# Performance work log

Hardware: AMD Instinct MI355X
Metric: run time of the kernel (lower is better)

## Reference

```python
import jax, jax.numpy as jnp
import numpy as np

THRESHOLD = 0.5
NEG_POS_RATIO = 3
ALPHA = 1.0
B, P, C, O = 64, 8732, 81, 32


def setup_inputs() -> dict:
    key = jax.random.key(0)
    k1, k2, k3, k4, k5, k6 = jax.random.split(key, 6)
    pred_locs = jax.random.normal(k1, (B, P, 4), dtype=jnp.float32)
    pred_scores = jax.random.normal(k2, (B, P, C), dtype=jnp.float32)
    # valid ground-truth corner boxes: sample center/size, convert to xy, clip to [0,1]
    ctr = jax.random.uniform(k3, (B, O, 2), minval=0.1, maxval=0.9)
    wh = jax.random.uniform(k4, (B, O, 2), minval=0.05, maxval=0.4)
    boxes = jnp.clip(jnp.concatenate([ctr - wh / 2, ctr + wh / 2], axis=-1), 0.0, 1.0)
    labels = jax.random.randint(k5, (B, O), 1, C, dtype=jnp.int64)
    pc = jax.random.uniform(k6, (P, 2), minval=0.05, maxval=0.95)
    pwh = jax.random.uniform(jax.random.fold_in(k6, 1), (P, 2), minval=0.05, maxval=0.3)
    priors_cxcy = jnp.concatenate([pc, pwh], axis=-1)
    return {"pred_locs": pred_locs, "pred_scores": pred_scores,
            "boxes": boxes, "labels": labels, "priors_cxcy": priors_cxcy}


def _jaccard(b, priors_xy):
    # b: [O,4] xy, priors_xy: [P,4] xy -> [O,P]
    lo = jnp.maximum(b[:, None, :2], priors_xy[None, :, :2])
    hi = jnp.minimum(b[:, None, 2:], priors_xy[None, :, 2:])
    inter = jnp.prod(jnp.clip(hi - lo, 0.0), axis=-1)
    area_b = jnp.prod(b[:, 2:] - b[:, :2], axis=-1)
    area_p = jnp.prod(priors_xy[:, 2:] - priors_xy[:, :2], axis=-1)
    return inter / (area_b[:, None] + area_p[None, :] - inter)


def _forward(pred_locs, pred_scores, boxes, labels, priors_cxcy):
    priors_xy = jnp.concatenate([priors_cxcy[:, :2] - priors_cxcy[:, 2:] / 2,
                                 priors_cxcy[:, :2] + priors_cxcy[:, 2:] / 2], axis=1)
    n_obj = boxes.shape[1]

    def match(b, l):
        ov = _jaccard(b, priors_xy)                      # [O,P]
        ov_fp = jnp.max(ov, axis=0)                      # [P]
        obj_fp = jnp.argmax(ov, axis=0)                  # [P]
        prior_fo = jnp.argmax(ov, axis=1)                # [O]
        obj_fp = obj_fp.at[prior_fo].set(jnp.arange(n_obj))
        ov_fp = ov_fp.at[prior_fo].set(1.0)
        lab = jnp.where(ov_fp < THRESHOLD, 0, l[obj_fp]) # [P]
        pt = b[obj_fp]                                   # [P,4] xy
        c = jnp.concatenate([(pt[:, 2:] + pt[:, :2]) / 2, pt[:, 2:] - pt[:, :2]], axis=1)
        g = jnp.concatenate([(c[:, :2] - priors_cxcy[:, :2]) / (priors_cxcy[:, 2:] / 10),
                             jnp.log(c[:, 2:] / priors_cxcy[:, 2:]) * 5], axis=1)
        return g, lab

    true_locs, true_classes = jax.vmap(match)(boxes, labels)  # [B,P,4], [B,P]

    pos = true_classes != 0                                   # [B,P]
    n_pos = jnp.sum(pos, axis=1)                              # [B]
    n_pos_total = jnp.sum(n_pos).astype(pred_locs.dtype)

    # L1Loss (mean over positive elements, 4 coords each)
    loc_abs = jnp.abs(pred_locs - true_locs) * pos[..., None].astype(pred_locs.dtype)
    loc_loss = jnp.sum(loc_abs) / (n_pos_total * 4.0)

    # per-prior cross entropy
    logp = jax.nn.log_softmax(pred_scores, axis=-1)           # [B,P,C]
    ce = -jnp.take_along_axis(logp, true_classes[..., None], axis=-1)[..., 0]  # [B,P]

    posf = pos.astype(ce.dtype)
    conf_pos_sum = jnp.sum(ce * posf)
    conf_neg = jnp.where(pos, 0.0, ce)
    conf_neg_sorted = -jnp.sort(-conf_neg, axis=1)            # descending
    ranks = jnp.arange(ce.shape[1])[None, :]
    hard = ranks < (NEG_POS_RATIO * n_pos)[:, None]
    conf_hard_neg_sum = jnp.sum(conf_neg_sorted * hard.astype(ce.dtype))

    conf_loss = (conf_hard_neg_sum + conf_pos_sum) / n_pos_total
    return conf_loss + ALPHA * loc_loss


def reference(pred_locs, pred_scores, boxes, labels, priors_cxcy):
    return _forward(pred_locs, pred_scores, boxes, labels, priors_cxcy)
```

## Files before the change

kernel.cpp:

```cpp
#include <hip/hip_runtime.h>

#define BB 64
#define PP 8732
#define OO 32
#define CC 81
#define NEGPOS 3
#define NSL_A 18
#define NCH_B 32
#define CHB 273
#define NSL_C 8
#define SLC 1092
#define NCE 8732

#define WS_POVF   0
#define WS_POVO   (WS_POVF  + BB*PP*4)
#define WS_BESTP  (WS_POVO  + BB*PP)
#define WS_LAB    (WS_BESTP + BB*NCH_B*OO*8)
#define WS_CENEG  (WS_LAB   + BB*PP)
#define WS_CEPOS  (WS_CENEG + BB*PP*4)
#define WS_LSUMB  (WS_CEPOS + NCE*4)
#define WS_NPOSB  (WS_LSUMB + BB*NSL_C*4)
#define WS_HARDB  (WS_NPOSB + BB*NSL_C*4)
#define WS_DONE   (WS_HARDB + BB*4)

__global__ __launch_bounds__(512) void match_geom(
    const float* __restrict__ boxes, const float* __restrict__ priors,
    float* __restrict__ povf, unsigned char* __restrict__ povo,
    unsigned long long* __restrict__ bestp, int* __restrict__ done)
{
    const int b = blockIdx.y, gx = blockIdx.x, tid = threadIdx.x;
    __shared__ float sbx[OO * 4];
    __shared__ unsigned long long sred[8 * OO];
    if (tid < OO * 4) sbx[tid] = boxes[b * OO * 4 + tid];
    if (gx == 0 && b == 0 && tid == 0) *done = 0;
    __syncthreads();

    if (gx < NSL_A) {
        const int p = gx * 512 + tid;
        if (p >= PP) return;
        float4 pr = ((const float4*)priors)[p];
        float plx = pr.x - pr.z * 0.5f, ply = pr.y - pr.w * 0.5f;
        float phx = pr.x + pr.z * 0.5f, phy = pr.y + pr.w * 0.5f;
        float parea = pr.z * pr.w;
        float bestv = -1.0f; int besto = 0;
#pragma unroll
        for (int o = 0; o < OO; ++o) {
            float b0 = sbx[o*4+0], b1 = sbx[o*4+1], b2 = sbx[o*4+2], b3 = sbx[o*4+3];
            float lox = fmaxf(b0, plx), loy = fmaxf(b1, ply);
            float hix = fminf(b2, phx), hiy = fminf(b3, phy);
            float inter = fmaxf(hix - lox, 0.0f) * fmaxf(hiy - loy, 0.0f);
            float iou = inter / ((b2 - b0) * (b3 - b1) + parea - inter);
            if (iou > bestv) { bestv = iou; besto = o; }
        }
        povf[b * PP + p] = bestv;
        povo[b * PP + p] = (unsigned char)besto;
    } else {
        const int ch = gx - NSL_A;
        const int o = tid & 31, sub = tid >> 5;
        const float b0 = sbx[o*4+0], b1 = sbx[o*4+1], b2 = sbx[o*4+2], b3 = sbx[o*4+3];
        const float barea = (b2 - b0) * (b3 - b1);
        const int base = ch * CHB;
        unsigned long long best = 0ull;
        for (int i = sub; i < CHB; i += 16) {
            int p = base + i;
            if (p >= PP) break;
            float4 pr = ((const float4*)priors)[p];
            float plx = pr.x - pr.z * 0.5f, ply = pr.y - pr.w * 0.5f;
            float phx = pr.x + pr.z * 0.5f, phy = pr.y + pr.w * 0.5f;
            float parea = pr.z * pr.w;
            float lox = fmaxf(b0, plx), loy = fmaxf(b1, ply);
            float hix = fminf(b2, phx), hiy = fminf(b3, phy);
            float inter = fmaxf(hix - lox, 0.0f) * fmaxf(hiy - loy, 0.0f);
            float iou = inter / (barea + parea - inter);
            unsigned long long enc =
                ((unsigned long long)__float_as_uint(iou) << 32) | (unsigned)(~(unsigned)p);
            best = (enc > best) ? enc : best;
        }
        unsigned long long w = __shfl_down(best, 32, 64);
        best = (w > best) ? w : best;
        const int wid = tid >> 6, lane = tid & 63;
        if (lane < 32) sred[wid * OO + o] = best;
        __syncthreads();
        if (tid < OO) {
            unsigned long long m = 0ull;
#pragma unroll
            for (int wv = 0; wv < 8; ++wv) {
                unsigned long long v = sred[wv * OO + tid];
                m = (v > m) ? v : m;
            }
            bestp[(b * NCH_B + ch) * OO + tid] = m;
        }
    }
}

__global__ __launch_bounds__(256) void match_b(
    const float* __restrict__ pred_locs, const float* __restrict__ boxes,
    const int* __restrict__ labels, const float* __restrict__ priors,
    const float* __restrict__ povf, const unsigned char* __restrict__ povo,
    const unsigned long long* __restrict__ bestp,
    signed char* __restrict__ lab_out, int* __restrict__ npos_bs,
    float* __restrict__ lsum_bs)
{
    const int b = blockIdx.y, sl = blockIdx.x, tid = threadIdx.x;
    const int base = sl * SLC;
    __shared__ float sbx[OO * 4];
    __shared__ int   slab[OO];
    __shared__ int   spfo[OO];
    __shared__ signed char sovr[SLC];
    __shared__ float sredf[4];
    __shared__ int   sredi[4];

    if (tid < OO * 4) sbx[tid] = boxes[b * OO * 4 + tid];
    if (tid < OO)     slab[tid] = labels[b * OO + tid];
    if (tid < OO) {
        unsigned long long m = 0ull;
        for (int c = 0; c < NCH_B; ++c) {
            unsigned long long v = bestp[(b * NCH_B + c) * OO + tid];
            m = (v > m) ? v : m;
        }
        spfo[tid] = (int)(~(unsigned)(m & 0xFFFFFFFFull));
    }
    for (int i = tid; i < SLC; i += 256) sovr[i] = -1;
    __syncthreads();
    if (tid == 0) {
        for (int o = 0; o < OO; ++o) {
            int p = spfo[o] - base;
            if (p >= 0 && p < SLC) sovr[p] = (signed char)o;
        }
    }
    __syncthreads();

    float lsum = 0.0f; int lpos = 0;
    for (int i = tid; i < SLC; i += 256) {
        int p = base + i;
        if (p >= PP) break;
        int o = (int)povo[b * PP + p];
        float ov = povf[b * PP + p];
        int ovr = sovr[i];
        if (ovr >= 0) { o = ovr; ov = 1.0f; }
        int l = (ov < 0.5f) ? 0 : slab[o];
        lab_out[b * PP + p] = (signed char)l;
        if (l != 0) {
            lpos++;
            float b0 = sbx[o*4+0], b1 = sbx[o*4+1], b2 = sbx[o*4+2], b3 = sbx[o*4+3];
            float4 pr = ((const float4*)priors)[p];
            float gx = ((b0 + b2) * 0.5f - pr.x) / (pr.z * 0.1f);
            float gy = ((b1 + b3) * 0.5f - pr.y) / (pr.w * 0.1f);
            float gw = logf((b2 - b0) / pr.z) * 5.0f;
            float gh = logf((b3 - b1) / pr.w) * 5.0f;
            float4 pl = ((const float4*)pred_locs)[b * PP + p];
            lsum += fabsf(pl.x - gx) + fabsf(pl.y - gy) + fabsf(pl.z - gw) + fabsf(pl.w - gh);
        }
    }
    for (int off = 32; off > 0; off >>= 1) {
        lsum += __shfl_down(lsum, off, 64);
        lpos += __shfl_down(lpos, off, 64);
    }
    if ((tid & 63) == 0) { sredf[tid >> 6] = lsum; sredi[tid >> 6] = lpos; }
    __syncthreads();
    if (tid == 0) {
        float s = 0.0f; int n = 0;
#pragma unroll
        for (int w = 0; w < 4; ++w) { s += sredf[w]; n += sredi[w]; }
        lsum_bs[b * NSL_C + sl] = s;
        npos_bs[b * NSL_C + sl] = n;
    }
}

__global__ __launch_bounds__(256) void ce_kernel(
    const float* __restrict__ scores, const signed char* __restrict__ lab,
    float* __restrict__ ce_neg, float* __restrict__ cepos)
{
    const int tid = threadIdx.x;
    const int g = tid >> 2, j = tid & 3;
    const int bp = blockIdx.x * 64 + g;
    const float* __restrict__ v = scores + (long long)bp * CC;
    const int l = (int)lab[bp];

    float d[21];
#pragma unroll
    for (int k = 0; k < 5; ++k) {
        const int c4 = (4 * k + j) * 4;
#pragma unroll
        for (int q = 0; q < 4; ++q) d[4*k+q] = v[c4 + q];
    }
    d[20] = (j == 0) ? v[80] : -3.0e38f;

    float m = d[20];
#pragma unroll
    for (int i = 0; i < 20; ++i) m = fmaxf(m, d[i]);
    m = fmaxf(m, __shfl_xor(m, 1, 64));
    m = fmaxf(m, __shfl_xor(m, 2, 64));

    float s = 0.0f;
#pragma unroll
    for (int i = 0; i < 21; ++i) s += __expf(d[i] - m);

    float vl = 0.0f;
    if (l == 80) { if (j == 0) vl = d[20]; }
    else { int c = l >> 2; if ((c & 3) == j) vl = d[4 * (c >> 2) + (l & 3)]; }

    s  += __shfl_xor(s, 1, 64);   s  += __shfl_xor(s, 2, 64);
    vl += __shfl_xor(vl, 1, 64);  vl += __shfl_xor(vl, 2, 64);

    float ce = m + __logf(s) - vl;
    if (j == 0) ce_neg[bp] = (l != 0) ? 0.0f : ce;
    float posc = (l != 0 && j == 0) ? ce : 0.0f;

    for (int off = 32; off > 0; off >>= 1) posc += __shfl_down(posc, off, 64);
    __shared__ float sr[4];
    if ((tid & 63) == 0) sr[tid >> 6] = posc;
    __syncthreads();
    if (tid == 0) cepos[blockIdx.x] = sr[0] + sr[1] + sr[2] + sr[3];
}

__global__ __launch_bounds__(512) void topk_kernel(
    const float* __restrict__ ce_neg, const int* __restrict__ npos_bs,
    const float* __restrict__ cepos, const float* __restrict__ lsum_bs,
    float* __restrict__ hard_b, int* __restrict__ done, float* __restrict__ out)
{
    __shared__ float sv[PP];
    __shared__ int hist[256 * 16];
    __shared__ int ssum[256];
    __shared__ unsigned sel[2];
    __shared__ float sr[8];
    __shared__ int sK;
    const int b = blockIdx.x, tid = threadIdx.x;
    for (int p = tid; p < PP; p += 512) sv[p] = ce_neg[b * PP + p];
    if (tid == 0) {
        int n = 0;
        for (int c = 0; c < NSL_C; ++c) n += npos_bs[b * NSL_C + c];
        int k = NEGPOS * n;
        sK = (k > PP) ? PP : k;
    }
    __syncthreads();
    const int K = sK;

    float hard = 0.0f;
    if (K > 0) {
        unsigned prefix = 0, mask = 0;
        unsigned remaining = (unsigned)K;
        for (int pass = 0; pass < 4; ++pass) {
            const int shift = 24 - 8 * pass;
            for (int i = tid; i < 256 * 16; i += 512) hist[i] = 0;
            __syncthreads();
            for (int p = tid; p < PP; p += 512) {
                unsigned u = __float_as_uint(sv[p]);
                if ((u & mask) == prefix)
                    atomicAdd(&hist[(((u >> shift) & 255) << 4) | (tid & 15)], 1);
            }
            __syncthreads();
            if (tid < 256) {
                int s = 0;
#pragma unroll
                for (int w = 0; w < 16; ++w) s += hist[(tid << 4) | w];
                ssum[tid] = s;
            }
            __syncthreads();
            for (int off = 1; off < 256; off <<= 1) {
                int vv = 0;
                if (tid < 256) vv = (tid + off < 256) ? ssum[tid + off] : 0;
                __syncthreads();
                if (tid < 256) ssum[tid] += vv;
                __syncthreads();
            }
            if (tid < 256 && (unsigned)ssum[tid] >= remaining &&
                (tid == 255 || (unsigned)ssum[tid + 1] < remaining)) {
                sel[0] = (unsigned)tid;
                sel[1] = remaining - ((tid == 255) ? 0u : (unsigned)ssum[tid + 1]);
            }
            __syncthreads();
            prefix |= sel[0] << shift;
            mask |= 0xFFu << shift;
            remaining = sel[1];
            __syncthreads();
        }
        float sgt = 0.0f;
        for (int p = tid; p < PP; p += 512) {
            unsigned u = __float_as_uint(sv[p]);
            if (u > prefix) sgt += sv[p];
        }
        for (int off = 32; off > 0; off >>= 1) sgt += __shfl_down(sgt, off, 64);
        if ((tid & 63) == 0) sr[tid >> 6] = sgt;
        __syncthreads();
        if (tid == 0) {
            hard = 0.0f;
#pragma unroll
            for (int w = 0; w < 8; ++w) hard += sr[w];
            hard += __uint_as_float(prefix) * (float)remaining;
        }
    }
    __shared__ int sticket;
    if (tid == 0) {
        hard_b[b] = hard;
        __threadfence();
        sticket = atomicAdd(done, 1);
    }
    __syncthreads();
    if (sticket != BB - 1) return;

    float cpos = 0.0f, labs = 0.0f, chard = 0.0f; int n = 0;
    for (int i = tid; i < NCE; i += 512) cpos += cepos[i];
    for (int i = tid; i < BB * NSL_C; i += 512) { labs += lsum_bs[i]; n += npos_bs[i]; }
    if (tid < BB) chard = atomicAdd(&hard_b[tid], 0.0f);
    for (int off = 32; off > 0; off >>= 1) {
        cpos  += __shfl_down(cpos, off, 64);
        labs  += __shfl_down(labs, off, 64);
        chard += __shfl_down(chard, off, 64);
        n     += __shfl_down(n, off, 64);
    }
    __shared__ float f0[8], f1[8], f2[8];
    __shared__ int i3[8];
    if ((tid & 63) == 0) { int w = tid >> 6; f0[w] = cpos; f1[w] = labs; f2[w] = chard; i3[w] = n; }
    __syncthreads();
    if (tid == 0) {
        float a = 0.0f, bs = 0.0f, c = 0.0f; int nt = 0;
#pragma unroll
        for (int w = 0; w < 8; ++w) { a += f0[w]; bs += f1[w]; c += f2[w]; nt += i3[w]; }
        float nf = (float)nt;
        out[0] = (c + a) / nf + bs / (nf * 4.0f);
    }
}

extern "C" void kernel_launch(void* const* d_in, const int* in_sizes, int n_in,
                              void* d_out, int out_size, void* d_ws, size_t ws_size,
                              hipStream_t stream) {
    const float* pred_locs   = (const float*)d_in[0];
    const float* pred_scores = (const float*)d_in[1];
    const float* boxes       = (const float*)d_in[2];
    const int*   labels      = (const int*)d_in[3];
    const float* priors      = (const float*)d_in[4];
    float* out = (float*)d_out;

    char* ws = (char*)d_ws;
    float* povf = (float*)(ws + WS_POVF);
    unsigned char* povo = (unsigned char*)(ws + WS_POVO);
    unsigned long long* bestp = (unsigned long long*)(ws + WS_BESTP);
    signed char* lab = (signed char*)(ws + WS_LAB);
    float* ce_neg  = (float*)(ws + WS_CENEG);
    float* cepos   = (float*)(ws + WS_CEPOS);
    float* lsum_bs = (float*)(ws + WS_LSUMB);
    int*   nposbs  = (int*)(ws + WS_NPOSB);
    float* hard_b  = (float*)(ws + WS_HARDB);
    int*   done    = (int*)(ws + WS_DONE);

    match_geom<<<dim3(NSL_A + NCH_B, BB), 512, 0, stream>>>(boxes, priors, povf, povo, bestp, done);
    match_b<<<dim3(NSL_C, BB), 256, 0, stream>>>(pred_locs, boxes, labels, priors,
                                                 povf, povo, bestp, lab, nposbs, lsum_bs);
    ce_kernel<<<NCE, 256, 0, stream>>>(pred_scores, lab, ce_neg, cepos);
    topk_kernel<<<BB, 512, 0, stream>>>(ce_neg, nposbs, cepos, lsum_bs, hard_b, done, out);
}
```

Measured before the change: 321.4 us.

## Fuse prior-label matching and loc loss into the cross-entropy kernel

Merges the match_b label/loc-loss kernel into the per-prior cross-entropy kernel, so each block handles 64 priors of one image. Labels are computed in registers, and the forced best-prior overrides are checked with a 32-way compare instead of a shared override table. This removes one launch and the byte label array round-trip through global memory. In exchange, every block re-reads the 32x32 bestp partials, and the final reduction handles more partial sums.

```diff
diff --git a/kernel.cpp b/kernel.cpp
--- a/kernel.cpp
+++ b/kernel.cpp
@@ -8,19 +8,16 @@
 #define NSL_A 18
 #define NCH_B 32
 #define CHB 273
-#define NSL_C 8
-#define SLC 1092
-#define NCE 8732
+#define NCEB 137
 
 #define WS_POVF   0
 #define WS_POVO   (WS_POVF  + BB*PP*4)
 #define WS_BESTP  (WS_POVO  + BB*PP)
-#define WS_LAB    (WS_BESTP + BB*NCH_B*OO*8)
-#define WS_CENEG  (WS_LAB   + BB*PP)
+#define WS_CENEG  (WS_BESTP + BB*NCH_B*OO*8)
 #define WS_CEPOS  (WS_CENEG + BB*PP*4)
-#define WS_LSUMB  (WS_CEPOS + NCE*4)
-#define WS_NPOSB  (WS_LSUMB + BB*NSL_C*4)
-#define WS_HARDB  (WS_NPOSB + BB*NSL_C*4)
+#define WS_LSUMB  (WS_CEPOS + BB*NCEB*4)
+#define WS_NPOSB  (WS_LSUMB + BB*NCEB*4)
+#define WS_HARDB  (WS_NPOSB + BB*NCEB*4)
 #define WS_DONE   (WS_HARDB + BB*4)
 
 __global__ __launch_bounds__(512) void match_geom(
@@ -93,130 +90,112 @@
     }
 }
 
-__global__ __launch_bounds__(256) void match_b(
-    const float* __restrict__ pred_locs, const float* __restrict__ boxes,
-    const int* __restrict__ labels, const float* __restrict__ priors,
+__global__ __launch_bounds__(256) void ce_match(
+    const float* __restrict__ scores, const float* __restrict__ pred_locs,
+    const float* __restrict__ boxes, const int* __restrict__ labels,
+    const float* __restrict__ priors,
     const float* __restrict__ povf, const unsigned char* __restrict__ povo,
     const unsigned long long* __restrict__ bestp,
-    signed char* __restrict__ lab_out, int* __restrict__ npos_bs,
-    float* __restrict__ lsum_bs)
+    float* __restrict__ ce_neg, float* __restrict__ cepos,
+    float* __restrict__ lsum_bc, int* __restrict__ npos_bc)
 {
-    const int b = blockIdx.y, sl = blockIdx.x, tid = threadIdx.x;
-    const int base = sl * SLC;
+    const int b = blockIdx.y, ch = blockIdx.x, tid = threadIdx.x;
+    const int base = ch * 64;
     __shared__ float sbx[OO * 4];
     __shared__ int   slab[OO];
     __shared__ int   spfo[OO];
-    __shared__ signed char sovr[SLC];
-    __shared__ float sredf[4];
-    __shared__ int   sredi[4];
+    __shared__ float srf[4], srl[4];
+    __shared__ int   sri[4];
 
     if (tid < OO * 4) sbx[tid] = boxes[b * OO * 4 + tid];
-    if (tid < OO)     slab[tid] = labels[b * OO + tid];
+    if (tid >= 224)   slab[tid - 224] = labels[b * OO + (tid - 224)];
     if (tid < OO) {
         unsigned long long m = 0ull;
+#pragma unroll 4
         for (int c = 0; c < NCH_B; ++c) {
             unsigned long long v = bestp[(b * NCH_B + c) * OO + tid];
             m = (v > m) ? v : m;
         }
         spfo[tid] = (int)(~(unsigned)(m & 0xFFFFFFFFull));
     }
-    for (int i = tid; i < SLC; i += 256) sovr[i] = -1;
-    __syncthreads();
-    if (tid == 0) {
-        for (int o = 0; o < OO; ++o) {
-            int p = spfo[o] - base;
-            if (p >= 0 && p < SLC) sovr[p] = (signed char)o;
-        }
-    }
-    __syncthreads();
-
-    float lsum = 0.0f; int lpos = 0;
-    for (int i = tid; i < SLC; i += 256) {
-        int p = base + i;
-        if (p >= PP) break;
-        int o = (int)povo[b * PP + p];
-        float ov = povf[b * PP + p];
-        int ovr = sovr[i];
-        if (ovr >= 0) { o = ovr; ov = 1.0f; }
-        int l = (ov < 0.5f) ? 0 : slab[o];
-        lab_out[b * PP + p] = (signed char)l;
-        if (l != 0) {
-            lpos++;
-            float b0 = sbx[o*4+0], b1 = sbx[o*4+1], b2 = sbx[o*4+2], b3 = sbx[o*4+3];
-            float4 pr = ((const float4*)priors)[p];
-            float gx = ((b0 + b2) * 0.5f - pr.x) / (pr.z * 0.1f);
-            float gy = ((b1 + b3) * 0.5f - pr.y) / (pr.w * 0.1f);
-            float gw = logf((b2 - b0) / pr.z) * 5.0f;
-            float gh = logf((b3 - b1) / pr.w) * 5.0f;
-            float4 pl = ((const float4*)pred_locs)[b * PP + p];
-            lsum += fabsf(pl.x - gx) + fabsf(pl.y - gy) + fabsf(pl.z - gw) + fabsf(pl.w - gh);
-        }
-    }
+    __syncthreads();
+
+    const int g = tid >> 2, j = tid & 3;
+    const int p = base + g;
+    float posc = 0.0f, lsum = 0.0f; int lpos = 0;
+
+    if (p < PP) {
+        const long long bp = (long long)b * PP + p;
+        const float* __restrict__ v = scores + bp * CC;
+
+        float d[21];
+#pragma unroll
+        for (int k = 0; k < 5; ++k) {
+            const int c4 = (4 * k + j) * 4;
+#pragma unroll
+            for (int q = 0; q < 4; ++q) d[4*k+q] = v[c4 + q];
+        }
+        d[20] = (j == 0) ? v[80] : -3.0e38f;
+
+        int o = (int)povo[bp];
+        float ov = povf[bp];
+#pragma unroll
+        for (int oo = 0; oo < OO; ++oo)
+            if (spfo[oo] == p) { o = oo; ov = 1.0f; }
+        const int l = (ov < 0.5f) ? 0 : slab[o];
+
+        float m = d[20];
+#pragma unroll
+        for (int i = 0; i < 20; ++i) m = fmaxf(m, d[i]);
+        m = fmaxf(m, __shfl_xor(m, 1, 64));
+        m = fmaxf(m, __shfl_xor(m, 2, 64));
+
+        float s = 0.0f;
+#pragma unroll
+        for (int i = 0; i < 21; ++i) s += __expf(d[i] - m);
+
+        float vl = 0.0f;
+        if (l == 80) { if (j == 0) vl = d[20]; }
+        else { int c = l >> 2; if ((c & 3) == j) vl = d[4 * (c >> 2) + (l & 3)]; }
+
+        s  += __shfl_xor(s, 1, 64);   s  += __shfl_xor(s, 2, 64);
+        vl += __shfl_xor(vl, 1, 64);  vl += __shfl_xor(vl, 2, 64);
+
+        float ce = m + __logf(s) - vl;
+        if (j == 0) {
+            ce_neg[bp] = (l != 0) ? 0.0f : ce;
+            if (l != 0) {
+                posc = ce; lpos = 1;
+                float b0 = sbx[o*4+0], b1 = sbx[o*4+1], b2 = sbx[o*4+2], b3 = sbx[o*4+3];
+                float4 pr = ((const float4*)priors)[p];
+                float gx = ((b0 + b2) * 0.5f - pr.x) / (pr.z * 0.1f);
+                float gy = ((b1 + b3) * 0.5f - pr.y) / (pr.w * 0.1f);
+                float gw = logf((b2 - b0) / pr.z) * 5.0f;
+                float gh = logf((b3 - b1) / pr.w) * 5.0f;
+                float4 pl = ((const float4*)pred_locs)[bp];
+                lsum = fabsf(pl.x - gx) + fabsf(pl.y - gy)
+                     + fabsf(pl.z - gw) + fabsf(pl.w - gh);
+            }
+        }
+    }
+
     for (int off = 32; off > 0; off >>= 1) {
+        posc += __shfl_down(posc, off, 64);
         lsum += __shfl_down(lsum, off, 64);
         lpos += __shfl_down(lpos, off, 64);
     }
-    if ((tid & 63) == 0) { sredf[tid >> 6] = lsum; sredi[tid >> 6] = lpos; }
+    if ((tid & 63) == 0) { int w = tid >> 6; srf[w] = posc; srl[w] = lsum; sri[w] = lpos; }
     __syncthreads();
     if (tid == 0) {
-        float s = 0.0f; int n = 0;
-#pragma unroll
-        for (int w = 0; w < 4; ++w) { s += sredf[w]; n += sredi[w]; }
-        lsum_bs[b * NSL_C + sl] = s;
-        npos_bs[b * NSL_C + sl] = n;
+        cepos[b * NCEB + ch]   = srf[0] + srf[1] + srf[2] + srf[3];
+        lsum_bc[b * NCEB + ch] = srl[0] + srl[1] + srl[2] + srl[3];
+        npos_bc[b * NCEB + ch] = sri[0] + sri[1] + sri[2] + sri[3];
     }
 }
 
-__global__ __launch_bounds__(256) void ce_kernel(
-    const float* __restrict__ scores, const signed char* __restrict__ lab,
-    float* __restrict__ ce_neg, float* __restrict__ cepos)
-{
-    const int tid = threadIdx.x;
-    const int g = tid >> 2, j = tid & 3;
-    const int bp = blockIdx.x * 64 + g;
-    const float* __restrict__ v = scores + (long long)bp * CC;
-    const int l = (int)lab[bp];
-
-    float d[21];
-#pragma unroll
-    for (int k = 0; k < 5; ++k) {
-        const int c4 = (4 * k + j) * 4;
-#pragma unroll
-        for (int q = 0; q < 4; ++q) d[4*k+q] = v[c4 + q];
-    }
-    d[20] = (j == 0) ? v[80] : -3.0e38f;
-
-    float m = d[20];
-#pragma unroll
-    for (int i = 0; i < 20; ++i) m = fmaxf(m, d[i]);
-    m = fmaxf(m, __shfl_xor(m, 1, 64));
-    m = fmaxf(m, __shfl_xor(m, 2, 64));
-
-    float s = 0.0f;
-#pragma unroll
-    for (int i = 0; i < 21; ++i) s += __expf(d[i] - m);
-
-    float vl = 0.0f;
-    if (l == 80) { if (j == 0) vl = d[20]; }
-    else { int c = l >> 2; if ((c & 3) == j) vl = d[4 * (c >> 2) + (l & 3)]; }
-
-    s  += __shfl_xor(s, 1, 64);   s  += __shfl_xor(s, 2, 64);
-    vl += __shfl_xor(vl, 1, 64);  vl += __shfl_xor(vl, 2, 64);
-
-    float ce = m + __logf(s) - vl;
-    if (j == 0) ce_neg[bp] = (l != 0) ? 0.0f : ce;
-    float posc = (l != 0 && j == 0) ? ce : 0.0f;
-
-    for (int off = 32; off > 0; off >>= 1) posc += __shfl_down(posc, off, 64);
-    __shared__ float sr[4];
-    if ((tid & 63) == 0) sr[tid >> 6] = posc;
-    __syncthreads();
-    if (tid == 0) cepos[blockIdx.x] = sr[0] + sr[1] + sr[2] + sr[3];
-}
-
 __global__ __launch_bounds__(512) void topk_kernel(
-    const float* __restrict__ ce_neg, const int* __restrict__ npos_bs,
-    const float* __restrict__ cepos, const float* __restrict__ lsum_bs,
+    const float* __restrict__ ce_neg, const int* __restrict__ npos_bc,
+    const float* __restrict__ cepos, const float* __restrict__ lsum_bc,
     float* __restrict__ hard_b, int* __restrict__ done, float* __restrict__ out)
 {
     __shared__ float sv[PP];
@@ -224,17 +203,25 @@
     __shared__ int ssum[256];
     __shared__ unsigned sel[2];
     __shared__ float sr[8];
-    __shared__ int sK;
+    __shared__ int sKred[8];
     const int b = blockIdx.x, tid = threadIdx.x;
     for (int p = tid; p < PP; p += 512) sv[p] = ce_neg[b * PP + p];
-    if (tid == 0) {
+
+    {
         int n = 0;
-        for (int c = 0; c < NSL_C; ++c) n += npos_bs[b * NSL_C + c];
-        int k = NEGPOS * n;
-        sK = (k > PP) ? PP : k;
-    }
-    __syncthreads();
-    const int K = sK;
+        for (int c = tid; c < NCEB; c += 512) n += npos_bc[b * NCEB + c];
+        for (int off = 32; off > 0; off >>= 1) n += __shfl_down(n, off, 64);
+        if ((tid & 63) == 0) sKred[tid >> 6] = n;
+    }
+    __syncthreads();
+    int K;
+    {
+        int n = 0;
+#pragma unroll
+        for (int w = 0; w < 8; ++w) n += sKred[w];
+        K = NEGPOS * n;
+        if (K > PP) K = PP;
+    }
 
     float hard = 0.0f;
     if (K > 0) {
@@ -300,8 +287,11 @@
     if (sticket != BB - 1) return;
 
     float cpos = 0.0f, labs = 0.0f, chard = 0.0f; int n = 0;
-    for (int i = tid; i < NCE; i += 512) cpos += cepos[i];
-    for (int i = tid; i < BB * NSL_C; i += 512) { labs += lsum_bs[i]; n += npos_bs[i]; }
+    for (int i = tid; i < BB * NCEB; i += 512) {
+        cpos += cepos[i];
+        labs += lsum_bc[i];
+        n    += npos_bc[i];
+    }
     if (tid < BB) chard = atomicAdd(&hard_b[tid], 0.0f);
     for (int off = 32; off > 0; off >>= 1) {
         cpos  += __shfl_down(cpos, off, 64);
@@ -336,17 +326,16 @@
     float* povf = (float*)(ws + WS_POVF);
     unsigned char* povo = (unsigned char*)(ws + WS_POVO);
     unsigned long long* bestp = (unsigned long long*)(ws + WS_BESTP);
-    signed char* lab = (signed char*)(ws + WS_LAB);
     float* ce_neg  = (float*)(ws + WS_CENEG);
     float* cepos   = (float*)(ws + WS_CEPOS);
-    float* lsum_bs = (float*)(ws + WS_LSUMB);
-    int*   nposbs  = (int*)(ws + WS_NPOSB);
+    float* lsum_bc = (float*)(ws + WS_LSUMB);
+    int*   nposbc  = (int*)(ws + WS_NPOSB);
     float* hard_b  = (float*)(ws + WS_HARDB);
     int*   done    = (int*)(ws + WS_DONE);
 
     match_geom<<<dim3(NSL_A + NCH_B, BB), 512, 0, stream>>>(boxes, priors, povf, povo, bestp, done);
-    match_b<<<dim3(NSL_C, BB), 256, 0, stream>>>(pred_locs, boxes, labels, priors,
-                                                 povf, povo, bestp, lab, nposbs, lsum_bs);
-    ce_kernel<<<NCE, 256, 0, stream>>>(pred_scores, lab, ce_neg, cepos);
-    topk_kernel<<<BB, 512, 0, stream>>>(ce_neg, nposbs, cepos, lsum_bs, hard_b, done, out);
+    ce_match<<<dim3(NCEB, BB), 256, 0, stream>>>(pred_scores, pred_locs, boxes, labels,
+                                                 priors, povf, povo, bestp,
+                                                 ce_neg, cepos, lsum_bc, nposbc);
+    topk_kernel<<<BB, 512, 0, stream>>>(ce_neg, nposbc, cepos, lsum_bc, hard_b, done, out);
 }
```

After: 318.8 us. Within noise of the previous version (-0.8%).
